# Kernel tuning notes

Hardware: AMD Instinct MI355X
Metric: run time of the kernel (lower is better)

## Reference

```python
import jax, jax.numpy as jnp
import numpy as np

C = 256
NH = 8
DH = C // NH
LN_EPS = 1e-5
COS_EPS = 1e-6


def _ln(x, w, b):
    m = x.mean(axis=-1, keepdims=True)
    v = ((x - m) ** 2).mean(axis=-1, keepdims=True)
    return (x - m) / jnp.sqrt(v + LN_EPS) * w + b


def _mha(q_in, kv_in, in_proj_w, in_proj_b, out_proj_w, out_proj_b):
    # q_in, kv_in: [P, S, C]. torch.nn.MultiheadAttention (batch_first).
    P, S, _ = q_in.shape
    q = q_in @ in_proj_w[:C].T + in_proj_b[:C]
    k = kv_in @ in_proj_w[C:2 * C].T + in_proj_b[C:2 * C]
    v = kv_in @ in_proj_w[2 * C:].T + in_proj_b[2 * C:]
    q = q.reshape(P, S, NH, DH)
    k = k.reshape(P, S, NH, DH)
    v = v.reshape(P, S, NH, DH)
    scores = jnp.einsum('pqhd,pkhd->phqk', q, k) / jnp.sqrt(jnp.asarray(DH, q.dtype))
    attn = jax.nn.softmax(scores, axis=-1)
    ctx = jnp.einsum('phqk,pkhd->pqhd', attn, v).reshape(P, S, C)
    return ctx @ out_proj_w.T + out_proj_b


def setup_inputs() -> dict:
    key = jax.random.key(0)
    ks = jax.random.split(key, 8)
    s = 0.02
    return {
        'z_sem': jax.random.normal(ks[0], (16, C, 32, 32), jnp.float32),
        'pair_indices': jnp.arange(16, dtype=jnp.int32).reshape(8, 2),
        'ln_w': jnp.ones((C,), jnp.float32),
        'ln_b': jnp.zeros((C,), jnp.float32),
        'in_proj_w': jax.random.normal(ks[1], (3 * C, C), jnp.float32) * s,
        'in_proj_b': jnp.zeros((3 * C,), jnp.float32),
        'out_proj_w': jax.random.normal(ks[2], (C, C), jnp.float32) * s,
        'out_proj_b': jnp.zeros((C,), jnp.float32),
        'res_scale': jnp.asarray(0.1, jnp.float32),
        'gate_scale': jnp.asarray(2.0, jnp.float32),
        'mlp_ln_w': jnp.ones((C,), jnp.float32),
        'mlp_ln_b': jnp.zeros((C,), jnp.float32),
        'mlp_w1': jax.random.normal(ks[3], (4 * C, C), jnp.float32) * s,
        'mlp_b1': jnp.zeros((4 * C,), jnp.float32),
        'mlp_w2': jax.random.normal(ks[4], (C, 4 * C), jnp.float32) * s,
        'mlp_b2': jnp.zeros((C,), jnp.float32),
    }


def reference(z_sem, pair_indices, ln_w, ln_b, in_proj_w, in_proj_b,
              out_proj_w, out_proj_b, res_scale, gate_scale,
              mlp_ln_w, mlp_ln_b, mlp_w1, mlp_b1, mlp_w2, mlp_b2):
    B, Cc, Hh, Ww = z_sem.shape
    S = Hh * Ww
    tokens = z_sem.reshape(B, Cc, S).transpose(0, 2, 1)  # [B, S, C]

    i_idx = pair_indices[:, 0]
    j_idx = pair_indices[:, 1]
    base_i = tokens[i_idx]  # [P, S, C]
    base_j = tokens[j_idx]

    q_i = _ln(base_i, ln_w, ln_b)
    q_j = _ln(base_j, ln_w, ln_b)

    cross_i = _mha(q_i, q_j, in_proj_w, in_proj_b, out_proj_w, out_proj_b)
    cross_j = _mha(q_j, q_i, in_proj_w, in_proj_b, out_proj_w, out_proj_b)

    # cosine similarity between mean-pooled normed tokens
    mi = q_i.mean(axis=1)  # [P, C]
    mj = q_j.mean(axis=1)
    ni = mi / jnp.maximum(jnp.linalg.norm(mi, axis=-1, keepdims=True), COS_EPS)
    nj = mj / jnp.maximum(jnp.linalg.norm(mj, axis=-1, keepdims=True), COS_EPS)
    sim = (ni * nj).sum(axis=-1)  # [P]
    gate = jax.nn.sigmoid(gate_scale * sim)  # [P]

    g = (res_scale * gate)[:, None, None]
    new_i = base_i + g * cross_i
    new_j = base_j + g * cross_j

    def _mlp(x):
        h = _ln(x, mlp_ln_w, mlp_ln_b)
        h = jax.nn.gelu(h @ mlp_w1.T + mlp_b1, approximate=False)
        return h @ mlp_w2.T + mlp_b2

    new_i = new_i + _mlp(new_i)
    new_j = new_j + _mlp(new_j)

    updated = tokens.at[i_idx].set(new_i).at[j_idx].set(new_j)
    shared = updated.transpose(0, 2, 1).reshape(B, Cc, Hh, Ww)
    return shared, gate, sim
```

## Files before the change

kernel.cpp:

```cpp
#include <hip/hip_runtime.h>
#include <hip/hip_bf16.h>

#define C_ 256
#define S_ 1024
#define NH_ 8
#define DH_ 32
#define NSIDE 16
#define MTOT (NSIDE * S_)

typedef __hip_bfloat16 bf16;
typedef short bf8_t __attribute__((ext_vector_type(8)));
typedef float f4_t __attribute__((ext_vector_type(4)));

#define SCALE2 0.25504167f

__device__ __forceinline__ float b2f(bf16 x) { return __bfloat162float(x); }
__device__ __forceinline__ bf16 f2b(float x) { return __float2bfloat16(x); }
__device__ __forceinline__ unsigned short f2bu(float x) {
    bf16 h = f2b(x);
    return *reinterpret_cast<unsigned short*>(&h);
}
__device__ __forceinline__ unsigned pack_trunc(float a, float b) {
    return (__float_as_uint(a) >> 16) | (__float_as_uint(b) & 0xFFFF0000u);
}

__device__ __forceinline__ float block_sum(float v, float* red) {
#pragma unroll
    for (int off = 1; off < 64; off <<= 1) v += __shfl_xor(v, off);
    __syncthreads();
    if ((threadIdx.x & 63) == 0) red[threadIdx.x >> 6] = v;
    __syncthreads();
    return red[0] + red[1] + red[2] + red[3];
}

__device__ __forceinline__ void packone(const float* __restrict__ src, bf16* __restrict__ dst,
                                        int i, int kshift) {
    int n = i >> kshift, k = i & ((1 << kshift) - 1);
    size_t a = ((size_t)((n >> 4) * (1 << (kshift - 5)) + (k >> 5)) << 9) +
               (((k >> 3) & 3) << 7) + ((n & 15) << 3) + (k & 7);
    dst[a] = f2b(src[i]);
}

__global__ void pack4(const float* __restrict__ a, bf16* __restrict__ oa,
                      const float* __restrict__ b, bf16* __restrict__ ob,
                      const float* __restrict__ c, bf16* __restrict__ oc,
                      const float* __restrict__ d, bf16* __restrict__ od) {
    int i = blockIdx.x * blockDim.x + threadIdx.x;
    if (i < 196608) { packone(a, oa, i, 8); return; }
    i -= 196608;
    if (i < 65536) { packone(b, ob, i, 8); return; }
    i -= 65536;
    if (i < 262144) { packone(c, oc, i, 8); return; }
    i -= 262144;
    if (i < 262144) packone(d, od, i, 10);
}

__global__ __launch_bounds__(256) void ln_tokens_g(const float* __restrict__ src,
                                                   const int* __restrict__ pair,
                                                   const float* __restrict__ w,
                                                   const float* __restrict__ b,
                                                   bf16* __restrict__ dst) {
    __shared__ float psum[4][64], psq[4][64], mean_s[64], rstd_s[64];
    __shared__ float wb[512];
    int sb = blockIdx.x, u = blockIdx.y;
    int bi = pair[u];
    int tid = threadIdx.x;
    wb[tid] = w[tid];
    wb[256 + tid] = b[tid];
    int sl = tid & 63, cp = tid >> 6;
    int s = sb * 64 + sl;
    const float* zb = src + (size_t)bi * C_ * S_ + s;
    float sum = 0.f, sq = 0.f;
    for (int c = cp * 64; c < cp * 64 + 64; ++c) {
        float x = zb[(size_t)c * S_];
        sum += x;
        sq += x * x;
    }
    psum[cp][sl] = sum;
    psq[cp][sl] = sq;
    __syncthreads();
    if (tid < 64) {
        float sm = psum[0][tid] + psum[1][tid] + psum[2][tid] + psum[3][tid];
        float q2 = psq[0][tid] + psq[1][tid] + psq[2][tid] + psq[3][tid];
        float mean = sm * (1.0f / C_);
        float var = q2 * (1.0f / C_) - mean * mean;
        mean_s[tid] = mean;
        rstd_s[tid] = rsqrtf(var + 1e-5f);
    }
    __syncthreads();
    float mean = mean_s[sl], rstd = rstd_s[sl];
    int m = u * S_ + s;
    size_t tile8 = (size_t)(m >> 4) * 8;
    for (int c8 = 0; c8 < 64; c8 += 8) {
        int c = cp * 64 + c8;
        bf8_t pk;
#pragma unroll
        for (int j = 0; j < 8; ++j) {
            float x = zb[(size_t)(c + j) * S_];
            float y = (x - mean) * rstd * wb[c + j] + wb[256 + c + j];
            pk[j] = (short)f2bu(y);
        }
        *reinterpret_cast<bf8_t*>(dst + ((tile8 + (c >> 5)) << 9) +
                                  (((c >> 3) & 3) << 7) + ((m & 15) << 3)) = pk;
    }
}

__global__ __launch_bounds__(256) void mean_partial(const bf16* __restrict__ qln,
                                                    float* __restrict__ partial) {
    int u = blockIdx.y, sy = blockIdx.x;
    int c = threadIdx.x;
    float sum = 0.f;
    int s0 = sy * 128;
    int inner = (((c >> 3) & 3) << 7) + (c & 7);
    for (int a = 0; a < 8; ++a) {
        const bf16* p = qln + ((((size_t)u * 64 + (s0 >> 4) + a) * 8 + (c >> 5)) << 9) + inner;
#pragma unroll
        for (int bq = 0; bq < 16; ++bq) sum += b2f(p[bq << 3]);
    }
    partial[(u * 8 + sy) * C_ + c] = sum;
}

__global__ __launch_bounds__(256) void gate_kernel(const float* __restrict__ partial,
                                                   const float* __restrict__ gate_scale,
                                                   float* __restrict__ gatef,
                                                   float* __restrict__ out_gate,
                                                   float* __restrict__ out_sim) {
    __shared__ float red[4];
    int p = blockIdx.x, c = threadIdx.x;
    float mi = 0.f, mj = 0.f;
    for (int sy = 0; sy < 8; ++sy) {
        mi += partial[((2 * p) * 8 + sy) * C_ + c];
        mj += partial[((2 * p + 1) * 8 + sy) * C_ + c];
    }
    mi *= (1.f / S_);
    mj *= (1.f / S_);
    float ii = block_sum(mi * mi, red);
    float jj = block_sum(mj * mj, red);
    float ij = block_sum(mi * mj, red);
    if (c == 0) {
        float ni = fmaxf(sqrtf(ii), 1e-6f);
        float nj = fmaxf(sqrtf(jj), 1e-6f);
        float sim = ij / (ni * nj);
        float gate = 1.f / (1.f + expf(-gate_scale[0] * sim));
        gatef[p] = gate;
        out_gate[p] = gate;
        out_sim[p] = sim;
    }
}

__global__ __launch_bounds__(256) void gemm_qkv(
    const bf16* __restrict__ Apk, const bf16* __restrict__ Wpk, const float* __restrict__ bias,
    bf16* __restrict__ qpk, bf16* __restrict__ kpk, bf16* __restrict__ vpk) {
    int tid = threadIdx.x;
    int wv = tid >> 6, lane = tid & 63;
    int ln15 = lane & 15, quad = lane >> 4;
    int idx = blockIdx.x * 4 + wv;
    int mt = idx / 12, nt = idx % 12;
    int m0 = mt * 64, n0 = nt * 64;

    f4_t acc[4][4];
#pragma unroll
    for (int i = 0; i < 4; ++i)
#pragma unroll
        for (int j = 0; j < 4; ++j) acc[i][j] = (f4_t)(0.0f);

    const bf16* Ab = Apk + ((size_t)mt << 14) + lane * 8;
    const bf16* Wb = Wpk + ((size_t)nt << 14) + lane * 8;

    bf8_t a0[4], w0[4], a1[4], w1[4];
#pragma unroll
    for (int i = 0; i < 4; ++i) {
        a0[i] = *reinterpret_cast<const bf8_t*>(Ab + ((size_t)(i * 8) << 9));
        w0[i] = *reinterpret_cast<const bf8_t*>(Wb + ((size_t)(i * 8) << 9));
    }
    for (int kch = 0; kch < 8; kch += 2) {
#pragma unroll
        for (int i = 0; i < 4; ++i) {
            a1[i] = *reinterpret_cast<const bf8_t*>(Ab + ((size_t)(i * 8 + kch + 1) << 9));
            w1[i] = *reinterpret_cast<const bf8_t*>(Wb + ((size_t)(i * 8 + kch + 1) << 9));
        }
#pragma unroll
        for (int i = 0; i < 4; ++i)
#pragma unroll
            for (int j = 0; j < 4; ++j)
                acc[i][j] = __builtin_amdgcn_mfma_f32_16x16x32_bf16(a0[i], w0[j], acc[i][j], 0, 0, 0);
        if (kch + 2 < 8) {
#pragma unroll
            for (int i = 0; i < 4; ++i) {
                a0[i] = *reinterpret_cast<const bf8_t*>(Ab + ((size_t)(i * 8 + kch + 2) << 9));
                w0[i] = *reinterpret_cast<const bf8_t*>(Wb + ((size_t)(i * 8 + kch + 2) << 9));
            }
        }
#pragma unroll
        for (int i = 0; i < 4; ++i)
#pragma unroll
            for (int j = 0; j < 4; ++j)
                acc[i][j] = __builtin_amdgcn_mfma_f32_16x16x32_bf16(a1[i], w1[j], acc[i][j], 0, 0, 0);
    }

#pragma unroll
    for (int i = 0; i < 4; ++i) {
#pragma unroll
        for (int j = 0; j < 4; ++j) {
            int coln = n0 + j * 16 + ln15;
            float bs = bias[coln];
            int row0 = m0 + i * 16 + quad * 4;
            int u = row0 >> 10, s0v = row0 & 1023;
            if (coln < 256) {
                int h = coln >> 5, d = coln & 31;
                bf16* qp = qpk + (((size_t)u * 8 + h) * 1024 + s0v) * 32 + d;
#pragma unroll
                for (int r = 0; r < 4; ++r)
                    qp[r * 32] = f2b((acc[i][j][r] + bs) * SCALE2);
            } else if (coln < 512) {
                int c = coln - 256, h = c >> 5, d = c & 31;
                bf16* kp = kpk + (((size_t)u * 8 + h) * 1024 + s0v) * 32 + d;
#pragma unroll
                for (int r = 0; r < 4; ++r)
                    kp[r * 32] = f2b(acc[i][j][r] + bs);
            } else {
                int c = coln - 512, h = c >> 5, d = c & 31;
                ushort4 pk;
#pragma unroll
                for (int r = 0; r < 4; ++r)
                    ((unsigned short*)&pk)[r] = f2bu(acc[i][j][r] + bs);
                *reinterpret_cast<ushort4*>(
                    vpk + ((((size_t)u * 8 + h) * 32 + (s0v >> 5)) * 32 + d) * 32 + (s0v & 31)) = pk;
            }
        }
    }
}

__global__ __launch_bounds__(256) void attn_mfma(const bf16* __restrict__ qpk,
                                                 const bf16* __restrict__ kpk,
                                                 const bf16* __restrict__ vpk,
                                                 bf16* __restrict__ ctx) {
    __shared__ __align__(16) short smem[4 * 1280];
    int tid = threadIdx.x;
    int wv = tid >> 6, lane = tid & 63;
    int ln15 = lane & 15, quad = lane >> 4;
    int h = blockIdx.y, u = blockIdx.z, up = u ^ 1;
    int q0 = blockIdx.x * 128 + wv * 32;
    short* PL = smem + wv * 1280;

    const bf16* Qb = qpk + ((size_t)u * 8 + h) * 1024 * 32;
    const bf16* Kb = kpk + ((size_t)up * 8 + h) * 1024 * 32;
    const bf16* Vb = vpk + ((size_t)up * 8 + h) * 1024 * 32;

    bf8_t qf[2];
#pragma unroll
    for (int qt = 0; qt < 2; ++qt)
        qf[qt] = *reinterpret_cast<const bf8_t*>(Qb + (size_t)(q0 + qt * 16 + ln15) * 32 + quad * 8);

    f4_t o[2][2];
#pragma unroll
    for (int i = 0; i < 2; ++i)
#pragma unroll
        for (int j = 0; j < 2; ++j) o[i][j] = (f4_t)(0.0f);
    float l[2] = {0.f, 0.f};

    for (int kt = 0; kt < 32; ++kt) {
        int k0 = kt * 32;
        bf8_t kf0 = *reinterpret_cast<const bf8_t*>(Kb + (size_t)(k0 + ln15) * 32 + quad * 8);
        bf8_t kf1 = *reinterpret_cast<const bf8_t*>(Kb + (size_t)(k0 + 16 + ln15) * 32 + quad * 8);
        bf8_t vt0 = *reinterpret_cast<const bf8_t*>(Vb + (size_t)kt * 1024 + ln15 * 32 + quad * 8);
        bf8_t vt1 = *reinterpret_cast<const bf8_t*>(Vb + (size_t)kt * 1024 + (16 + ln15) * 32 + quad * 8);

        f4_t zf = (f4_t)(0.0f);
        f4_t st[2][2];
#pragma unroll
        for (int qt = 0; qt < 2; ++qt) {
            st[0][qt] = __builtin_amdgcn_mfma_f32_16x16x32_bf16(kf0, qf[qt], zf, 0, 0, 0);
            st[1][qt] = __builtin_amdgcn_mfma_f32_16x16x32_bf16(kf1, qf[qt], zf, 0, 0, 0);
        }

#pragma unroll
        for (int qt = 0; qt < 2; ++qt) {
#pragma unroll
            for (int kh = 0; kh < 2; ++kh) {
                float e0 = exp2f(st[kh][qt][0]);
                float e1 = exp2f(st[kh][qt][1]);
                float e2 = exp2f(st[kh][qt][2]);
                float e3 = exp2f(st[kh][qt][3]);
                l[qt] += (e0 + e1) + (e2 + e3);
                uint2 pk;
                pk.x = pack_trunc(e0, e1);
                pk.y = pack_trunc(e2, e3);
                *reinterpret_cast<uint2*>(PL + qt * 640 + ln15 * 40 + kh * 16 + quad * 4) = pk;
            }
        }
#pragma unroll
        for (int qt = 0; qt < 2; ++qt) {
            bf8_t pf = *reinterpret_cast<const bf8_t*>(PL + qt * 640 + ln15 * 40 + quad * 8);
            o[0][qt] = __builtin_amdgcn_mfma_f32_16x16x32_bf16(vt0, pf, o[0][qt], 0, 0, 0);
            o[1][qt] = __builtin_amdgcn_mfma_f32_16x16x32_bf16(vt1, pf, o[1][qt], 0, 0, 0);
        }
    }

#pragma unroll
    for (int qt = 0; qt < 2; ++qt) {
        l[qt] += __shfl_xor(l[qt], 16);
        l[qt] += __shfl_xor(l[qt], 32);
    }

#pragma unroll
    for (int qt = 0; qt < 2; ++qt) {
        float inv = 1.f / l[qt];
        size_t base = ((size_t)(u * S_ + q0 + qt * 16 + ln15)) * C_ + h * DH_;
#pragma unroll
        for (int dh = 0; dh < 2; ++dh) {
            ushort4 pk;
            pk.x = f2bu(o[dh][qt][0] * inv);
            pk.y = f2bu(o[dh][qt][1] * inv);
            pk.z = f2bu(o[dh][qt][2] * inv);
            pk.w = f2bu(o[dh][qt][3] * inv);
            *reinterpret_cast<ushort4*>(ctx + base + dh * 16 + quad * 4) = pk;
        }
    }
}

__global__ __launch_bounds__(512) void fused_tail(
    const bf16* __restrict__ ctx, const bf16* __restrict__ wout,
    const float* __restrict__ bout, const float* __restrict__ z,
    const int* __restrict__ pair, const float* __restrict__ gatef,
    const float* __restrict__ res_scale,
    const float* __restrict__ lnw, const float* __restrict__ lnb,
    const bf16* __restrict__ w1b, const float* __restrict__ b1,
    const bf16* __restrict__ w2b, const float* __restrict__ b2,
    float* __restrict__ outp) {
    __shared__ __align__(16) short Xs[32][264];
    __shared__ __align__(16) short CHs[32][264];
    __shared__ float ssum[8][32], ssq[8][32], smean[32], srstd[32];

    int tid = threadIdx.x;
    int wv = tid >> 6, lane = tid & 63;
    int ln15 = lane & 15, quad = lane >> 4;
    int u = blockIdx.x >> 5;
    int s0 = (blockIdx.x & 31) * 32;
    int bi = pair[u];
    float g = res_scale[0] * gatef[u >> 1];
    int c0 = wv * 32;

    {
        int row = tid >> 4, col = (tid & 15) * 16;
        const bf16* src = ctx + ((size_t)(u * S_ + s0 + row)) * 256 + col;
        *reinterpret_cast<bf8_t*>(&CHs[row][col]) = *reinterpret_cast<const bf8_t*>(src);
        *reinterpret_cast<bf8_t*>(&CHs[row][col + 8]) = *reinterpret_cast<const bf8_t*>(src + 8);
    }
    __syncthreads();

    f4_t yacc[2][2];
#pragma unroll
    for (int i = 0; i < 2; ++i)
#pragma unroll
        for (int j = 0; j < 2; ++j) yacc[i][j] = (f4_t)(0.0f);
    {
        const bf16* Wb = wout + (((size_t)(wv * 2) * 8) << 9) + lane * 8;
#pragma unroll
        for (int kch = 0; kch < 8; ++kch) {
            bf8_t wf[2], xf[2];
#pragma unroll
            for (int i = 0; i < 2; ++i)
                wf[i] = *reinterpret_cast<const bf8_t*>(Wb + ((size_t)(i * 8 + kch) << 9));
#pragma unroll
            for (int j = 0; j < 2; ++j)
                xf[j] = *reinterpret_cast<const bf8_t*>(&CHs[j * 16 + ln15][kch * 32 + quad * 8]);
#pragma unroll
            for (int i = 0; i < 2; ++i)
#pragma unroll
                for (int j = 0; j < 2; ++j)
                    yacc[i][j] = __builtin_amdgcn_mfma_f32_16x16x32_bf16(wf[i], xf[j], yacc[i][j], 0, 0, 0);
        }
    }
    float psum[2] = {0.f, 0.f}, psq[2] = {0.f, 0.f};
#pragma unroll
    for (int i = 0; i < 2; ++i) {
#pragma unroll
        for (int r = 0; r < 4; ++r) {
            int c = c0 + i * 16 + quad * 4 + r;
            float bs = bout[c];
            const float* zr = z + ((size_t)bi * C_ + c) * S_ + s0;
#pragma unroll
            for (int j = 0; j < 2; ++j) {
                int sl = j * 16 + ln15;
                float y = zr[sl] + g * (yacc[i][j][r] + bs);
                yacc[i][j][r] = y;
                psum[j] += y;
                psq[j] += y * y;
            }
        }
    }
#pragma unroll
    for (int j = 0; j < 2; ++j) {
        psum[j] += __shfl_xor(psum[j], 16);
        psum[j] += __shfl_xor(psum[j], 32);
        psq[j] += __shfl_xor(psq[j], 16);
        psq[j] += __shfl_xor(psq[j], 32);
    }
    if (quad == 0) {
#pragma unroll
        for (int j = 0; j < 2; ++j) {
            ssum[wv][j * 16 + ln15] = psum[j];
            ssq[wv][j * 16 + ln15] = psq[j];
        }
    }
    __syncthreads();
    if (tid < 32) {
        float sm = 0.f, q2 = 0.f;
#pragma unroll
        for (int w = 0; w < 8; ++w) {
            sm += ssum[w][tid];
            q2 += ssq[w][tid];
        }
        float mean = sm * (1.0f / C_);
        float var = q2 * (1.0f / C_) - mean * mean;
        smean[tid] = mean;
        srstd[tid] = rsqrtf(var + 1e-5f);
    }
    __syncthreads();
#pragma unroll
    for (int j = 0; j < 2; ++j) {
        int sl = j * 16 + ln15;
        float mean = smean[sl], rstd = srstd[sl];
#pragma unroll
        for (int i = 0; i < 2; ++i) {
            ushort4 pk;
#pragma unroll
            for (int r = 0; r < 4; ++r) {
                int c = c0 + i * 16 + quad * 4 + r;
                float xv = (yacc[i][j][r] - mean) * rstd * lnw[c] + lnb[c];
                ((unsigned short*)&pk)[r] = f2bu(xv);
            }
            *reinterpret_cast<ushort4*>(&Xs[sl][c0 + i * 16 + quad * 4]) = pk;
        }
    }
    __syncthreads();

    f4_t acc2[2][2];
#pragma unroll
    for (int i = 0; i < 2; ++i)
#pragma unroll
        for (int j = 0; j < 2; ++j) acc2[i][j] = (f4_t)(0.0f);

    for (int pass = 0; pass < 4; ++pass) {
        f4_t hacc[2][2];
#pragma unroll
        for (int i = 0; i < 2; ++i)
#pragma unroll
            for (int j = 0; j < 2; ++j) hacc[i][j] = (f4_t)(0.0f);
        {
            const bf16* W1p = w1b + (((size_t)(pass * 16 + wv * 2) * 8) << 9) + lane * 8;
#pragma unroll
            for (int kch = 0; kch < 8; ++kch) {
                bf8_t wf[2], xf[2];
#pragma unroll
                for (int i = 0; i < 2; ++i)
                    wf[i] = *reinterpret_cast<const bf8_t*>(W1p + ((size_t)(i * 8 + kch) << 9));
#pragma unroll
                for (int j = 0; j < 2; ++j)
                    xf[j] = *reinterpret_cast<const bf8_t*>(&Xs[j * 16 + ln15][kch * 32 + quad * 8]);
#pragma unroll
                for (int i = 0; i < 2; ++i)
#pragma unroll
                    for (int j = 0; j < 2; ++j)
                        hacc[i][j] = __builtin_amdgcn_mfma_f32_16x16x32_bf16(wf[i], xf[j], hacc[i][j], 0, 0, 0);
            }
        }
#pragma unroll
        for (int j = 0; j < 2; ++j) {
#pragma unroll
            for (int i = 0; i < 2; ++i) {
                ushort4 pk;
#pragma unroll
                for (int r = 0; r < 4; ++r) {
                    int hg = pass * 256 + c0 + i * 16 + quad * 4 + r;
                    float v = hacc[i][j][r] + b1[hg];
                    float ge = 0.5f * v * (1.f + erff(v * 0.70710678118f));
                    ((unsigned short*)&pk)[r] = f2bu(ge);
                }
                *reinterpret_cast<ushort4*>(&CHs[j * 16 + ln15][c0 + i * 16 + quad * 4]) = pk;
            }
        }
        __syncthreads();
        {
            const bf16* W2p = w2b + (((size_t)(wv * 2) * 32 + pass * 8) << 9) + lane * 8;
#pragma unroll
            for (int kch = 0; kch < 8; ++kch) {
                bf8_t wf[2], hf[2];
#pragma unroll
                for (int i = 0; i < 2; ++i)
                    wf[i] = *reinterpret_cast<const bf8_t*>(W2p + ((size_t)(i * 32 + kch) << 9));
#pragma unroll
                for (int j = 0; j < 2; ++j)
                    hf[j] = *reinterpret_cast<const bf8_t*>(&CHs[j * 16 + ln15][kch * 32 + quad * 8]);
#pragma unroll
                for (int i = 0; i < 2; ++i)
#pragma unroll
                    for (int j = 0; j < 2; ++j)
                        acc2[i][j] = __builtin_amdgcn_mfma_f32_16x16x32_bf16(wf[i], hf[j], acc2[i][j], 0, 0, 0);
            }
        }
        __syncthreads();
    }

#pragma unroll
    for (int i = 0; i < 2; ++i) {
#pragma unroll
        for (int r = 0; r < 4; ++r) {
            int c = c0 + i * 16 + quad * 4 + r;
            float bs = b2[c];
            float* orow = outp + ((size_t)bi * C_ + c) * S_ + s0;
#pragma unroll
            for (int j = 0; j < 2; ++j)
                orow[j * 16 + ln15] = yacc[i][j][r] + acc2[i][j][r] + bs;
        }
    }
}

extern "C" void kernel_launch(void* const* d_in, const int* in_sizes, int n_in,
                              void* d_out, int out_size, void* d_ws, size_t ws_size,
                              hipStream_t stream) {
    const float* z = (const float*)d_in[0];
    const int* pair = (const int*)d_in[1];
    const float* ln_w = (const float*)d_in[2];
    const float* ln_b = (const float*)d_in[3];
    const float* in_proj_w = (const float*)d_in[4];
    const float* in_proj_b = (const float*)d_in[5];
    const float* out_proj_w = (const float*)d_in[6];
    const float* out_proj_b = (const float*)d_in[7];
    const float* res_scale = (const float*)d_in[8];
    const float* gate_scale = (const float*)d_in[9];
    const float* mlp_ln_w = (const float*)d_in[10];
    const float* mlp_ln_b = (const float*)d_in[11];
    const float* mlp_w1 = (const float*)d_in[12];
    const float* mlp_b1 = (const float*)d_in[13];
    const float* mlp_w2 = (const float*)d_in[14];
    const float* mlp_b2 = (const float*)d_in[15];
    float* out = (float*)d_out;

    char* ws = (char*)d_ws;
    bf16* qln = (bf16*)(ws);
    bf16* qpk = (bf16*)(ws + 8388608);
    bf16* kpk = (bf16*)(ws + 16777216);
    bf16* vpk = (bf16*)(ws + 25165824);
    bf16* ctx = (bf16*)(ws + 33554432);
    bf16* wqkv = (bf16*)(ws + 41943040);
    bf16* wout = (bf16*)(ws + 41943040 + 393216);
    bf16* w1b = (bf16*)(ws + 41943040 + 524288);
    bf16* w2b = (bf16*)(ws + 41943040 + 1048576);
    float* partial = (float*)(ws + 50331648);
    float* gatef = (float*)(ws + 50462720);

    pack4<<<3072, 256, 0, stream>>>(in_proj_w, wqkv, out_proj_w, wout,
                                    mlp_w1, w1b, mlp_w2, w2b);
    ln_tokens_g<<<dim3(16, 16), 256, 0, stream>>>(z, pair, ln_w, ln_b, qln);
    mean_partial<<<dim3(8, 16), 256, 0, stream>>>(qln, partial);
    gate_kernel<<<8, 256, 0, stream>>>(partial, gate_scale, gatef, out + 4194304, out + 4194312);
    gemm_qkv<<<768, 256, 0, stream>>>(qln, wqkv, in_proj_b, qpk, kpk, vpk);
    attn_mfma<<<dim3(8, 8, 16), 256, 0, stream>>>(qpk, kpk, vpk, ctx);
    fused_tail<<<512, 512, 0, stream>>>(ctx, wout, out_proj_b, z, pair, gatef, res_scale,
                                        mlp_ln_w, mlp_ln_b, w1b, mlp_b1, w2b, mlp_b2, out);
}
```

Baseline: 222.1 us.

## Unroll attention key loop to 64 keys, remap blocks for XCD locality

The attention kernel now processes 64 keys per iteration instead of 32, issuing four K loads and four V loads up front so more memory latency is hidden per loop trip, and the per-wave P staging buffer grows to match. The 3D grid is flattened to 1D with an index mapping that places all query blocks of one (pair-side, head) on the same XCD, so the shared K/V data stays in that XCD's L2. The bf16 truncation packing uses a single byte-permute instruction instead of shift and mask. The cost is higher register and LDS use per block, which may lower occupancy.

```diff
diff --git a/kernel.cpp b/kernel.cpp
--- a/kernel.cpp
+++ b/kernel.cpp
@@ -21,7 +21,7 @@
     return *reinterpret_cast<unsigned short*>(&h);
 }
 __device__ __forceinline__ unsigned pack_trunc(float a, float b) {
-    return (__float_as_uint(a) >> 16) | (__float_as_uint(b) & 0xFFFF0000u);
+    return __builtin_amdgcn_perm(__float_as_uint(b), __float_as_uint(a), 0x07060302u);
 }
 
 __device__ __forceinline__ float block_sum(float v, float* red) {
@@ -235,49 +235,63 @@
                                                  const bf16* __restrict__ kpk,
                                                  const bf16* __restrict__ vpk,
                                                  bf16* __restrict__ ctx) {
-    __shared__ __align__(16) short smem[4 * 1280];
+    __shared__ __align__(16) short smem[4 * 2304];
     int tid = threadIdx.x;
     int wv = tid >> 6, lane = tid & 63;
     int ln15 = lane & 15, quad = lane >> 4;
-    int h = blockIdx.y, u = blockIdx.z, up = u ^ 1;
-    int q0 = blockIdx.x * 128 + wv * 32;
-    short* PL = smem + wv * 1280;
-
-    const bf16* Qb = qpk + ((size_t)u * 8 + h) * 1024 * 32;
-    const bf16* Kb = kpk + ((size_t)up * 8 + h) * 1024 * 32;
-    const bf16* Vb = vpk + ((size_t)up * 8 + h) * 1024 * 32;
+    int bid = blockIdx.x;
+    int g = bid >> 6, rem = bid & 63;
+    int qb = rem >> 3, xcd = rem & 7;
+    int uh = g * 8 + xcd;
+    int u = uh >> 3, h = uh & 7, up = u ^ 1;
+    int q0 = qb * 128 + wv * 32;
+    short* PL = smem + wv * 2304;
+
+    const bf16* Qb = qpk + (size_t)uh * 32768;
+    const bf16* Kb = kpk + ((size_t)(up * 8 + h)) * 32768;
+    const bf16* Vb = vpk + ((size_t)(up * 8 + h)) * 32768;
 
     bf8_t qf[2];
 #pragma unroll
     for (int qt = 0; qt < 2; ++qt)
         qf[qt] = *reinterpret_cast<const bf8_t*>(Qb + (size_t)(q0 + qt * 16 + ln15) * 32 + quad * 8);
 
+    const bf16* kp = Kb + ln15 * 32 + quad * 8;
+    const bf16* vp = Vb + ln15 * 32 + quad * 8;
+    short* plw = PL + ln15 * 72 + quad * 4;
+    const short* plr = PL + ln15 * 72 + quad * 8;
+
     f4_t o[2][2];
 #pragma unroll
     for (int i = 0; i < 2; ++i)
 #pragma unroll
         for (int j = 0; j < 2; ++j) o[i][j] = (f4_t)(0.0f);
     float l[2] = {0.f, 0.f};
-
-    for (int kt = 0; kt < 32; ++kt) {
-        int k0 = kt * 32;
-        bf8_t kf0 = *reinterpret_cast<const bf8_t*>(Kb + (size_t)(k0 + ln15) * 32 + quad * 8);
-        bf8_t kf1 = *reinterpret_cast<const bf8_t*>(Kb + (size_t)(k0 + 16 + ln15) * 32 + quad * 8);
-        bf8_t vt0 = *reinterpret_cast<const bf8_t*>(Vb + (size_t)kt * 1024 + ln15 * 32 + quad * 8);
-        bf8_t vt1 = *reinterpret_cast<const bf8_t*>(Vb + (size_t)kt * 1024 + (16 + ln15) * 32 + quad * 8);
-
-        f4_t zf = (f4_t)(0.0f);
-        f4_t st[2][2];
+    f4_t zf = (f4_t)(0.0f);
+
+    for (int it = 0; it < 16; ++it) {
+        int k0 = it * 64;
+        bf8_t kf[4], vt[2][2];
+#pragma unroll
+        for (int t = 0; t < 4; ++t)
+            kf[t] = *reinterpret_cast<const bf8_t*>(kp + (size_t)(k0 + t * 16) * 32);
+#pragma unroll
+        for (int kc = 0; kc < 2; ++kc)
+#pragma unroll
+            for (int dh = 0; dh < 2; ++dh)
+                vt[kc][dh] = *reinterpret_cast<const bf8_t*>(vp + (size_t)(it * 2 + kc) * 1024 + dh * 512);
+
+        f4_t st[4][2];
+#pragma unroll
+        for (int kh = 0; kh < 4; ++kh)
+#pragma unroll
+            for (int qt = 0; qt < 2; ++qt)
+                st[kh][qt] = __builtin_amdgcn_mfma_f32_16x16x32_bf16(kf[kh], qf[qt], zf, 0, 0, 0);
+
 #pragma unroll
         for (int qt = 0; qt < 2; ++qt) {
-            st[0][qt] = __builtin_amdgcn_mfma_f32_16x16x32_bf16(kf0, qf[qt], zf, 0, 0, 0);
-            st[1][qt] = __builtin_amdgcn_mfma_f32_16x16x32_bf16(kf1, qf[qt], zf, 0, 0, 0);
-        }
-
-#pragma unroll
-        for (int qt = 0; qt < 2; ++qt) {
-#pragma unroll
-            for (int kh = 0; kh < 2; ++kh) {
+#pragma unroll
+            for (int kh = 0; kh < 4; ++kh) {
                 float e0 = exp2f(st[kh][qt][0]);
                 float e1 = exp2f(st[kh][qt][1]);
                 float e2 = exp2f(st[kh][qt][2]);
@@ -286,14 +300,17 @@
                 uint2 pk;
                 pk.x = pack_trunc(e0, e1);
                 pk.y = pack_trunc(e2, e3);
-                *reinterpret_cast<uint2*>(PL + qt * 640 + ln15 * 40 + kh * 16 + quad * 4) = pk;
+                *reinterpret_cast<uint2*>(plw + qt * 1152 + kh * 16) = pk;
             }
         }
 #pragma unroll
         for (int qt = 0; qt < 2; ++qt) {
-            bf8_t pf = *reinterpret_cast<const bf8_t*>(PL + qt * 640 + ln15 * 40 + quad * 8);
-            o[0][qt] = __builtin_amdgcn_mfma_f32_16x16x32_bf16(vt0, pf, o[0][qt], 0, 0, 0);
-            o[1][qt] = __builtin_amdgcn_mfma_f32_16x16x32_bf16(vt1, pf, o[1][qt], 0, 0, 0);
+#pragma unroll
+            for (int kc = 0; kc < 2; ++kc) {
+                bf8_t pf = *reinterpret_cast<const bf8_t*>(plr + qt * 1152 + kc * 32);
+                o[0][qt] = __builtin_amdgcn_mfma_f32_16x16x32_bf16(vt[kc][0], pf, o[0][qt], 0, 0, 0);
+                o[1][qt] = __builtin_amdgcn_mfma_f32_16x16x32_bf16(vt[kc][1], pf, o[1][qt], 0, 0, 0);
+            }
         }
     }
 
@@ -557,7 +574,7 @@
     mean_partial<<<dim3(8, 16), 256, 0, stream>>>(qln, partial);
     gate_kernel<<<8, 256, 0, stream>>>(partial, gate_scale, gatef, out + 4194304, out + 4194312);
     gemm_qkv<<<768, 256, 0, stream>>>(qln, wqkv, in_proj_b, qpk, kpk, vpk);
-    attn_mfma<<<dim3(8, 8, 16), 256, 0, stream>>>(qpk, kpk, vpk, ctx);
+    attn_mfma<<<1024, 256, 0, stream>>>(qpk, kpk, vpk, ctx);
     fused_tail<<<512, 512, 0, stream>>>(ctx, wout, out_proj_b, z, pair, gatef, res_scale,
                                         mlp_ln_w, mlp_ln_b, w1b, mlp_b1, w2b, mlp_b2, out);
 }
```

Result: no change. 223.9 us (+0.8%).
